# Performance work log

Measured on AMD Instinct MI355X. Metric: run time of the kernel, lower is better.

## Reference

```python
import jax, jax.numpy as jnp
import numpy as np

HIDDEN = 256
HORIZON = 24
FMET = 16
OUT = 1
EPS = 1e-5


def setup_inputs() -> dict:
    key = jax.random.key(0)
    ks = jax.random.split(key, 12)
    B, N = 16, 1000
    final_h = jax.random.normal(ks[0], (B, N, HIDDEN), dtype=jnp.float32)
    future_met = jax.random.normal(ks[1], (B, HORIZON, N, FMET), dtype=jnp.float32)
    # step_queries: xavier_uniform over (max_horizon, hidden)
    lim_q = float(np.sqrt(6.0 / (HORIZON + HIDDEN)))
    step_queries = jax.random.uniform(ks[2], (HORIZON, HIDDEN), minval=-lim_q, maxval=lim_q, dtype=jnp.float32)
    # future_met_proj: Linear(FMET -> HIDDEN); store weight as (FMET, HIDDEN)
    lim_fm = float(np.sqrt(1.0 / FMET))
    W_fm = jax.random.uniform(ks[3], (FMET, HIDDEN), minval=-lim_fm, maxval=lim_fm, dtype=jnp.float32)
    b_fm = jax.random.uniform(ks[4], (HIDDEN,), minval=-lim_fm, maxval=lim_fm, dtype=jnp.float32)
    gamma = jnp.ones((HIDDEN,), dtype=jnp.float32)
    beta = jnp.zeros((HIDDEN,), dtype=jnp.float32)
    lim1 = float(np.sqrt(1.0 / HIDDEN))
    W1 = jax.random.uniform(ks[5], (HIDDEN, HIDDEN), minval=-lim1, maxval=lim1, dtype=jnp.float32)
    b1 = jax.random.uniform(ks[6], (HIDDEN,), minval=-lim1, maxval=lim1, dtype=jnp.float32)
    W2 = jax.random.uniform(ks[7], (HIDDEN, OUT), minval=-lim1, maxval=lim1, dtype=jnp.float32)
    b2 = jax.random.uniform(ks[8], (OUT,), minval=-lim1, maxval=lim1, dtype=jnp.float32)
    return {
        "final_h": final_h,
        "future_met": future_met,
        "step_queries": step_queries,
        "W_fm": W_fm,
        "b_fm": b_fm,
        "gamma": gamma,
        "beta": beta,
        "W1": W1,
        "b1": b1,
        "W2": W2,
        "b2": b2,
    }


def _layer_norm(x, gamma, beta):
    mu = jnp.mean(x, axis=-1, keepdims=True)
    var = jnp.mean(jnp.square(x - mu), axis=-1, keepdims=True)
    return (x - mu) * jax.lax.rsqrt(var + EPS) * gamma + beta


def reference(final_h, future_met, step_queries, W_fm, b_fm, gamma, beta, W1, b1, W2, b2):
    # final_h: (B, N, H); future_met: (B, T, N, F)
    # combined: (B, N, T, H) = broadcast(final_h) + queries + proj(future_met)
    combined = final_h[:, :, None, :] + step_queries[None, None, :, :]
    fm = jnp.transpose(future_met, (0, 2, 1, 3))  # (B, N, T, F)
    combined = combined + (jnp.einsum("bntf,fh->bnth", fm, W_fm) + b_fm)
    x = _layer_norm(combined, gamma, beta)
    x = jax.nn.gelu(x @ W1 + b1, approximate=False)
    # dropout is identity in eval mode
    out = x @ W2 + b2  # (B, N, T, OUT)
    return jnp.transpose(out, (0, 2, 1, 3))  # (B, T, N, OUT)
```

## Files before the change

### kernel.cpp

```cpp
#include <hip/hip_runtime.h>
#include <hip/hip_bf16.h>
#include <stdint.h>

#define MROWS 32
#define LDA   264
#define FMS   40

typedef __bf16 bf16x8 __attribute__((ext_vector_type(8)));
typedef float  f32x4  __attribute__((ext_vector_type(4)));
typedef float  f32x2  __attribute__((ext_vector_type(2)));

__device__ __forceinline__ unsigned short f2bf(float f) {
    union { float f; uint32_t u; } v; v.f = f;
    return (unsigned short)((v.u + 0x7FFFu + ((v.u >> 16) & 1u)) >> 16);
}

__device__ __forceinline__ ushort2 pk_bf16(float a, float b) {
    union { __hip_bfloat162 v; ushort2 u; } c;
    c.v = __float22bfloat162_rn(make_float2(a, b));
    return c.u;
}

template <int CTRL>
__device__ __forceinline__ float dpp_radd(float x) {
    union { float f; int i; } a, b;
    a.f = x;
    b.i = __builtin_amdgcn_update_dpp(0, a.i, CTRL, 0xF, 0xF, true);
    return x + b.f;
}
#define ROW_SHR1 0x111
#define ROW_SHR2 0x112
#define ROW_SHR4 0x114
#define ROW_SHR8 0x118
__device__ __forceinline__ float dpp_rowsum(float x) {
    x = dpp_radd<ROW_SHR1>(x);
    x = dpp_radd<ROW_SHR2>(x);
    x = dpp_radd<ROW_SHR4>(x);
    x = dpp_radd<ROW_SHR8>(x);
    return x;
}

__device__ __forceinline__ f32x2 gelu_fast2(f32x2 v) {
    const f32x2 t = v * v;
    f32x2 p = t * 0.044715f + 1.0f;
    const f32x2 u = v * p;
    f32x2 e;
    e.x = __builtin_amdgcn_exp2f(u.x * -2.3021131160186336f);
    e.y = __builtin_amdgcn_exp2f(u.y * -2.3021131160186336f);
    f32x2 r;
    r.x = __builtin_amdgcn_rcpf(1.0f + e.x);
    r.y = __builtin_amdgcn_rcpf(1.0f + e.y);
    return v * r;
}

__device__ __forceinline__ int frag_n(int f) {
    return (f & 0xC0) | ((f & 3) << 4) | ((f >> 2) & 15);
}

__global__ __launch_bounds__(256) void prep1(const float* __restrict__ W1,
                                             const float* __restrict__ step_q,
                                             const float* __restrict__ b_fm,
                                             const float* __restrict__ W_fm,
                                             const float* __restrict__ gamma,
                                             const float* __restrict__ beta,
                                             unsigned short* __restrict__ w1frag,
                                             float* __restrict__ sqb,
                                             unsigned short* __restrict__ wfmfrag,
                                             float* __restrict__ gpart,
                                             float* __restrict__ bpart,
                                             float* __restrict__ WFWp,
                                             float* __restrict__ SQWp) {
    __shared__ unsigned short T[256][40];
    __shared__ float redw[8][32][41];
    const int blk = blockIdx.x, tid = threadIdx.x;
    if (blk < 8) {
        const int kk = blk;
        float sg = 0.f, sb = 0.f;
        #pragma unroll
        for (int r = 0; r < 32; ++r) {
            const int klog = frag_n((kk << 5) + r);
            const float wv = W1[klog * 256 + tid];
            const float gv = gamma[klog];
            sg = fmaf(gv, wv, sg);
            sb = fmaf(beta[klog], wv, sb);
            T[tid][r] = f2bf(wv * gv);
        }
        gpart[(kk << 8) + tid] = sg;
        bpart[(kk << 8) + tid] = sb;
        __syncthreads();
        #pragma unroll
        for (int f = 0; f < 4; ++f) {
            const int fi = (f << 8) + tid;
            const int l = fi & 63, j = (fi >> 6) & 3, w = fi >> 8;
            const int n = (w << 6) + (j << 4) + (l & 15);
            const uint4 v = *(const uint4*)&T[n][(l >> 4) << 3];
            *(uint4*)&w1frag[((w << 5) + (j << 3) + kk) * 512 + (l << 3)] = v;
        }
    } else if (blk < 32) {
        const int t = blk - 8;
        const int n = frag_n(tid);
        sqb[t * 256 + tid] = step_q[t * 256 + n] + b_fm[n];
    } else if (blk < 36) {
        const int f  = blk - 32;
        const int fr = (f << 8) + tid;
        const int l = fr & 63, j = (fr >> 6) & 3, w = fr >> 8;
        const int n = (w << 6) + (j << 4) + (l & 15);
        const int qr = l >> 4;
        #pragma unroll
        for (int e = 0; e < 8; ++e) {
            const int k = (qr << 3) + e;
            wfmfrag[(fr << 3) + e] = (k < 16) ? f2bf(W_fm[(k << 8) + n]) : (unsigned short)0;
        }
    } else {
        const int kc = tid >> 5, cl = tid & 31;
        const int n  = ((blk - 36) << 5) + cl;
        float wfw[16];
        float sqw[24];
        #pragma unroll
        for (int f = 0; f < 16; ++f) wfw[f] = 0.f;
        #pragma unroll
        for (int t = 0; t < 24; ++t) sqw[t] = 0.f;
        for (int hh = 0; hh < 32; ++hh) {
            const int h = (kc << 5) + hh;
            const float g1 = gamma[h] * W1[(h << 8) + n];
            #pragma unroll
            for (int f = 0; f < 16; ++f)
                wfw[f] = fmaf(W_fm[(f << 8) + h], g1, wfw[f]);
            const float bf = b_fm[h];
            #pragma unroll
            for (int t = 0; t < 24; ++t)
                sqw[t] = fmaf(step_q[(t << 8) + h] + bf, g1, sqw[t]);
        }
        #pragma unroll
        for (int f = 0; f < 16; ++f) redw[kc][cl][f] = wfw[f];
        #pragma unroll
        for (int t = 0; t < 24; ++t) redw[kc][cl][16 + t] = sqw[t];
        __syncthreads();
        for (int e = tid; e < 1280; e += 256) {
            const int cl2 = e & 31, v = e >> 5;
            float s = 0.f;
            #pragma unroll
            for (int k2 = 0; k2 < 8; ++k2) s += redw[k2][cl2][v];
            const int nn = ((blk - 36) << 5) + cl2;
            if (v < 16) WFWp[(v << 8) + nn] = s;
            else        SQWp[((v - 16) << 8) + nn] = s;
        }
    }
}

__global__ __launch_bounds__(256) void prep2(const float* __restrict__ gpart,
                                             const float* __restrict__ bpart,
                                             const float* __restrict__ b1,
                                             const float* __restrict__ W2,
                                             float* __restrict__ gw1f,
                                             float* __restrict__ b1tf,
                                             float* __restrict__ w2f) {
    const int tid = threadIdx.x;
    const int n = frag_n(tid);
    float sg = 0.f, sb = 0.f;
    #pragma unroll
    for (int kk = 0; kk < 8; ++kk) {
        sg += gpart[(kk << 8) + n];
        sb += bpart[(kk << 8) + n];
    }
    gw1f[tid] = sg;
    b1tf[tid] = sb + b1[n];
    w2f[tid]  = W2[n];
}

__global__ __launch_bounds__(256) void prep3(const float* __restrict__ final_h,
                                             const unsigned short* __restrict__ w1frag,
                                             const float* __restrict__ gpart,
                                             const float* __restrict__ bpart,
                                             const float* __restrict__ b1,
                                             const float* __restrict__ W2,
                                             const float* __restrict__ WFWp,
                                             const float* __restrict__ SQWp,
                                             float* __restrict__ gw1f,
                                             float* __restrict__ b1tf,
                                             float* __restrict__ w2f,
                                             unsigned short* __restrict__ wfwfrag,
                                             float* __restrict__ sqwf,
                                             float* __restrict__ FHW) {
    __shared__ __align__(16) unsigned short Abuf[MROWS * LDA];
    const int blk = blockIdx.x, tid = threadIdx.x;
    if (blk == 500) {
        const int n = frag_n(tid);
        float sg = 0.f, sb = 0.f;
        #pragma unroll
        for (int kk = 0; kk < 8; ++kk) {
            sg += gpart[(kk << 8) + n];
            sb += bpart[(kk << 8) + n];
        }
        gw1f[tid] = sg;
        b1tf[tid] = sb + b1[n];
        w2f[tid]  = W2[n];
        #pragma unroll
        for (int f = 0; f < 4; ++f) {
            const int fr = (f << 8) + tid;
            const int l = fr & 63, j = (fr >> 6) & 3, wq = fr >> 8;
            const int nn = (wq << 6) + (j << 4) + (l & 15);
            const int qr2 = l >> 4;
            #pragma unroll
            for (int e = 0; e < 8; ++e) {
                const int k = (qr2 << 3) + e;
                wfwfrag[(fr << 3) + e] = (k < 16) ? f2bf(WFWp[(k << 8) + nn]) : (unsigned short)0;
            }
        }
        #pragma unroll
        for (int t = 0; t < 24; ++t)
            sqwf[(t << 8) + tid] = SQWp[(t << 8) + n];
        return;
    }
    const int w = tid >> 6, l = tid & 63;
    const int col = l & 15, qr = l >> 4;
    const int fb = (w << 6) + (col << 2);
    const int R0 = blk << 5;
    #pragma unroll
    for (int i = 0; i < 2; ++i) {
        #pragma unroll
        for (int r = 0; r < 4; ++r) {
            const int m = (i << 4) + (qr << 2) + r;
            const float* src = final_h + ((R0 + m) << 8) + (w << 6) + col;
            const ushort2 p01 = pk_bf16(src[0],  src[16]);
            const ushort2 p23 = pk_bf16(src[32], src[48]);
            ushort4 o; o.x = p01.x; o.y = p01.y; o.z = p23.x; o.w = p23.y;
            *(ushort4*)&Abuf[m * LDA + fb] = o;
        }
    }
    __syncthreads();
    f32x4 acc[2][4];
    #pragma unroll
    for (int i = 0; i < 2; ++i)
        #pragma unroll
        for (int j = 0; j < 4; ++j)
            acc[i][j] = (f32x4){0.f, 0.f, 0.f, 0.f};
    {
        const unsigned short* Bw  = w1frag + (w << 14) + (l << 3);
        const unsigned short* Ab0 = &Abuf[col * LDA + (qr << 3)];
        const unsigned short* Ab1 = &Abuf[(16 + col) * LDA + (qr << 3)];
        #pragma unroll
        for (int kk = 0; kk < 8; ++kk) {
            const bf16x8 a0 = *(const bf16x8*)(Ab0 + (kk << 5));
            const bf16x8 a1 = *(const bf16x8*)(Ab1 + (kk << 5));
            #pragma unroll
            for (int j = 0; j < 4; ++j) {
                const bf16x8 bf = *(const bf16x8*)(Bw + (j << 12) + (kk << 9));
                acc[0][j] = __builtin_amdgcn_mfma_f32_16x16x32_bf16(a0, bf, acc[0][j], 0, 0, 0);
                acc[1][j] = __builtin_amdgcn_mfma_f32_16x16x32_bf16(a1, bf, acc[1][j], 0, 0, 0);
            }
        }
    }
    #pragma unroll
    for (int i = 0; i < 2; ++i) {
        #pragma unroll
        for (int r = 0; r < 4; ++r) {
            const int m = (i << 4) + (qr << 2) + r;
            float4 st;
            st.x = acc[i][0][r]; st.y = acc[i][1][r];
            st.z = acc[i][2][r]; st.w = acc[i][3][r];
            *(float4*)&FHW[((R0 + m) << 8) + fb] = st;
        }
    }
}

__global__ __launch_bounds__(256, 6) void fused_head(
    const float* __restrict__ final_h, const float* __restrict__ future_met,
    const float* __restrict__ b2,      const float* __restrict__ sqb,
    const unsigned short* __restrict__ wfmfrag,
    const float* __restrict__ gw1f,    const float* __restrict__ b1tf,
    const float* __restrict__ w2f,     const unsigned short* __restrict__ wfwfrag,
    const float* __restrict__ sqwf,    const float* __restrict__ FHW,
    float* __restrict__ out)
{
    __shared__ __align__(16) unsigned short fmA[MROWS * FMS];
    __shared__ float2 red[4][MROWS];
    __shared__ float2 mv[MROWS];
    __shared__ float  part[4][MROWS];

    const int tid = threadIdx.x;
    const int w   = tid >> 6;
    const int l   = tid & 63;
    const int col = l & 15;
    const int qr  = l >> 4;
    const int m0  = blockIdx.x * MROWS;
    const int bn0 = m0 / 24;
    const int tt0 = m0 - bn0 * 24;
    const int fb  = (w << 6) + (col << 2);

    if (tid < 128) {
        const int row = tid >> 2, f0 = (tid & 3) << 2;
        const int tta = tt0 + row;
        const int sub = (tta >= 24) + (tta >= 48);
        const int tt  = tta - sub * 24;
        const int bn  = bn0 + sub;
        const int b   = bn / 1000, n = bn - b * 1000;
        const float4 v = *(const float4*)&future_met[((((b * 24 + tt) * 1000) + n) << 4) + f0];
        ushort2 lo = pk_bf16(v.x, v.y), hi = pk_bf16(v.z, v.w);
        ushort4 o; o.x = lo.x; o.y = lo.y; o.z = hi.x; o.w = hi.y;
        *(ushort4*)&fmA[row * FMS + f0] = o;
    }
    {
        const int row = tid >> 3, k = 16 + ((tid & 7) << 1);
        *(unsigned int*)&fmA[row * FMS + k] = 0u;
    }
    __syncthreads();

    const int dlo = qr << 2;
    const int slo = ((tt0 + dlo) >= 24) + ((tt0 + dlo) >= 48);
    const int shi = ((tt0 + dlo + 19) >= 24) + ((tt0 + dlo + 19) >= 48);
    float flo[4], fhi[4];
    {
        const float* fhl = final_h + ((bn0 + slo) << 8) + (w << 6) + col;
        const float* fhh = final_h + ((bn0 + shi) << 8) + (w << 6) + col;
        #pragma unroll
        for (int j = 0; j < 4; ++j) { flo[j] = fhl[j << 4]; fhi[j] = fhh[j << 4]; }
    }

    f32x4 acc[2][4];
    #pragma unroll
    for (int i = 0; i < 2; ++i) {
        #pragma unroll
        for (int r = 0; r < 4; ++r) {
            const int d   = (i << 4) + (qr << 2) + r;
            const int tta = tt0 + d;
            const int sub = (tta >= 24) + (tta >= 48);
            const int tt  = tta - sub * 24;
            const bool lo = (sub == slo);
            const float4 sb4 = *(const float4*)&sqb[(tt << 8) + fb];
            acc[i][0][r] = (lo ? flo[0] : fhi[0]) + sb4.x;
            acc[i][1][r] = (lo ? flo[1] : fhi[1]) + sb4.y;
            acc[i][2][r] = (lo ? flo[2] : fhi[2]) + sb4.z;
            acc[i][3][r] = (lo ? flo[3] : fhi[3]) + sb4.w;
        }
    }
    const bf16x8 af0 = *(const bf16x8*)&fmA[col * FMS + (qr << 3)];
    const bf16x8 af1 = *(const bf16x8*)&fmA[(16 + col) * FMS + (qr << 3)];
    {
        const unsigned short* Bwf = wfmfrag + (w << 11) + (l << 3);
        #pragma unroll
        for (int j = 0; j < 4; ++j) {
            const bf16x8 bf = *(const bf16x8*)(Bwf + (j << 9));
            acc[0][j] = __builtin_amdgcn_mfma_f32_16x16x32_bf16(af0, bf, acc[0][j], 0, 0, 0);
            acc[1][j] = __builtin_amdgcn_mfma_f32_16x16x32_bf16(af1, bf, acc[1][j], 0, 0, 0);
        }
    }

    #pragma unroll
    for (int i = 0; i < 2; ++i) {
        #pragma unroll
        for (int r = 0; r < 4; ++r) {
            const int m = (i << 4) + (qr << 2) + r;
            const f32x2 vA = {acc[i][0][r], acc[i][1][r]};
            const f32x2 vB = {acc[i][2][r], acc[i][3][r]};
            const f32x2 sv = vA + vB;
            const f32x2 qv = vA * vA + vB * vB;
            float s = sv.x + sv.y;
            float q = qv.x + qv.y;
            s = dpp_rowsum(s);
            q = dpp_rowsum(q);
            if (col == 15) red[w][m] = make_float2(s, q);
        }
    }
    __syncthreads();

    if (tid < MROWS) {
        const float2 a0 = red[0][tid], a1 = red[1][tid], a2 = red[2][tid], a3 = red[3][tid];
        const float S = a0.x + a1.x + a2.x + a3.x;
        const float Q = a0.y + a1.y + a2.y + a3.y;
        const float mu = S * 0.00390625f;
        const float rstd = rsqrtf(Q * 0.00390625f - mu * mu + 1e-5f);
        mv[tid] = make_float2(mu, rstd);
    }

    #pragma unroll
    for (int i = 0; i < 2; ++i) {
        #pragma unroll
        for (int r = 0; r < 4; ++r) {
            const int d   = (i << 4) + (qr << 2) + r;
            const int tta = tt0 + d;
            const int sub = (tta >= 24) + (tta >= 48);
            const int tt  = tta - sub * 24;
            const float4 fw = *(const float4*)&FHW[((bn0 + sub) << 8) + fb];
            const float4 sw = *(const float4*)&sqwf[(tt << 8) + fb];
            acc[i][0][r] = fw.x + sw.x;
            acc[i][1][r] = fw.y + sw.y;
            acc[i][2][r] = fw.z + sw.z;
            acc[i][3][r] = fw.w + sw.w;
        }
    }
    {
        const unsigned short* Bw2 = wfwfrag + (w << 11) + (l << 3);
        #pragma unroll
        for (int j = 0; j < 4; ++j) {
            const bf16x8 bfv = *(const bf16x8*)(Bw2 + (j << 9));
            acc[0][j] = __builtin_amdgcn_mfma_f32_16x16x32_bf16(af0, bfv, acc[0][j], 0, 0, 0);
            acc[1][j] = __builtin_amdgcn_mfma_f32_16x16x32_bf16(af1, bfv, acc[1][j], 0, 0, 0);
        }
    }

    const float4 gw4 = *(const float4*)&gw1f[fb];
    const float4 bt4 = *(const float4*)&b1tf[fb];
    const float4 w24 = *(const float4*)&w2f[fb];
    const f32x2 gwA = {gw4.x, gw4.y}, gwB = {gw4.z, gw4.w};
    const f32x2 btA = {bt4.x, bt4.y}, btB = {bt4.z, bt4.w};
    const f32x2 w2A = {w24.x, w24.y}, w2B = {w24.z, w24.w};
    __syncthreads();

    #pragma unroll
    for (int i = 0; i < 2; ++i) {
        #pragma unroll
        for (int r = 0; r < 4; ++r) {
            const int m = (i << 4) + (qr << 2) + r;
            const float2 p = mv[m];
            const float cm = -p.x * p.y;
            const f32x2 baseA = gwA * cm + btA;
            const f32x2 baseB = gwB * cm + btB;
            const f32x2 accA = {acc[i][0][r], acc[i][1][r]};
            const f32x2 accB = {acc[i][2][r], acc[i][3][r]};
            const f32x2 yA = accA * p.y + baseA;
            const f32x2 yB = accB * p.y + baseB;
            const f32x2 gvA = gelu_fast2(yA);
            const f32x2 gvB = gelu_fast2(yB);
            const f32x2 pp2 = gvA * w2A + gvB * w2B;
            float pp = pp2.x + pp2.y;
            pp = dpp_rowsum(pp);
            if (col == 15) part[w][m] = pp;
        }
    }
    __syncthreads();

    if (tid < MROWS) {
        const int m = m0 + tid;
        const float val = part[0][tid] + part[1][tid] + part[2][tid] + part[3][tid] + b2[0];
        const int bn = m / 24, tt = m - bn * 24;
        const int b  = bn / 1000, n = bn - b * 1000;
        out[(b * 24 + tt) * 1000 + n] = val;
    }
}

__global__ __launch_bounds__(256, 6) void fused_head_v3(
    const float* __restrict__ final_h, const float* __restrict__ future_met,
    const float* __restrict__ b2,      const unsigned short* __restrict__ w1frag,
    const float* __restrict__ sqb,     const unsigned short* __restrict__ wfmfrag,
    const float* __restrict__ gw1f,    const float* __restrict__ b1tf,
    const float* __restrict__ w2f,     float* __restrict__ out)
{
    __shared__ __align__(16) unsigned short Abuf[MROWS * LDA];
    __shared__ __align__(16) unsigned short fmA[MROWS * FMS];
    __shared__ float2 red[4][MROWS];
    __shared__ float2 mv[MROWS];
    __shared__ float  part[4][MROWS];

    const int tid = threadIdx.x;
    const int w   = tid >> 6;
    const int l   = tid & 63;
    const int col = l & 15;
    const int qr  = l >> 4;
    const int m0  = blockIdx.x * MROWS;
    const int bn0 = m0 / 24;
    const int tt0 = m0 - bn0 * 24;
    const int fb  = (w << 6) + (col << 2);

    if (tid < 128) {
        const int row = tid >> 2, f0 = (tid & 3) << 2;
        const int tta = tt0 + row;
        const int sub = (tta >= 24) + (tta >= 48);
        const int tt  = tta - sub * 24;
        const int bn  = bn0 + sub;
        const int b   = bn / 1000, n = bn - b * 1000;
        const float4 v = *(const float4*)&future_met[((((b * 24 + tt) * 1000) + n) << 4) + f0];
        ushort2 lo = pk_bf16(v.x, v.y), hi = pk_bf16(v.z, v.w);
        ushort4 o; o.x = lo.x; o.y = lo.y; o.z = hi.x; o.w = hi.y;
        *(ushort4*)&fmA[row * FMS + f0] = o;
    }
    {
        const int row = tid >> 3, k = 16 + ((tid & 7) << 1);
        *(unsigned int*)&fmA[row * FMS + k] = 0u;
    }
    __syncthreads();

    const int dlo = qr << 2;
    const int slo = ((tt0 + dlo) >= 24) + ((tt0 + dlo) >= 48);
    const int shi = ((tt0 + dlo + 19) >= 24) + ((tt0 + dlo + 19) >= 48);
    float flo[4], fhi[4];
    {
        const float* fhl = final_h + ((bn0 + slo) << 8) + (w << 6) + col;
        const float* fhh = final_h + ((bn0 + shi) << 8) + (w << 6) + col;
        #pragma unroll
        for (int j = 0; j < 4; ++j) { flo[j] = fhl[j << 4]; fhi[j] = fhh[j << 4]; }
    }

    f32x4 acc[2][4];
    #pragma unroll
    for (int i = 0; i < 2; ++i) {
        #pragma unroll
        for (int r = 0; r < 4; ++r) {
            const int d   = (i << 4) + (qr << 2) + r;
            const int tta = tt0 + d;
            const int sub = (tta >= 24) + (tta >= 48);
            const int tt  = tta - sub * 24;
            const bool lo = (sub == slo);
            const float4 sb4 = *(const float4*)&sqb[(tt << 8) + fb];
            acc[i][0][r] = (lo ? flo[0] : fhi[0]) + sb4.x;
            acc[i][1][r] = (lo ? flo[1] : fhi[1]) + sb4.y;
            acc[i][2][r] = (lo ? flo[2] : fhi[2]) + sb4.z;
            acc[i][3][r] = (lo ? flo[3] : fhi[3]) + sb4.w;
        }
    }
    {
        const bf16x8 af0 = *(const bf16x8*)&fmA[col * FMS + (qr << 3)];
        const bf16x8 af1 = *(const bf16x8*)&fmA[(16 + col) * FMS + (qr << 3)];
        const unsigned short* Bwf = wfmfrag + (w << 11) + (l << 3);
        #pragma unroll
        for (int j = 0; j < 4; ++j) {
            const bf16x8 bf = *(const bf16x8*)(Bwf + (j << 9));
            acc[0][j] = __builtin_amdgcn_mfma_f32_16x16x32_bf16(af0, bf, acc[0][j], 0, 0, 0);
            acc[1][j] = __builtin_amdgcn_mfma_f32_16x16x32_bf16(af1, bf, acc[1][j], 0, 0, 0);
        }
    }

    #pragma unroll
    for (int i = 0; i < 2; ++i) {
        #pragma unroll
        for (int r = 0; r < 4; ++r) {
            const int m = (i << 4) + (qr << 2) + r;
            const f32x2 vA = {acc[i][0][r], acc[i][1][r]};
            const f32x2 vB = {acc[i][2][r], acc[i][3][r]};
            const f32x2 sv = vA + vB;
            const f32x2 qv = vA * vA + vB * vB;
            float s = sv.x + sv.y;
            float q = qv.x + qv.y;
            const ushort2 p01 = pk_bf16(vA.x, vA.y);
            const ushort2 p23 = pk_bf16(vB.x, vB.y);
            s = dpp_rowsum(s);
            q = dpp_rowsum(q);
            if (col == 15) red[w][m] = make_float2(s, q);
            ushort4 o; o.x = p01.x; o.y = p01.y; o.z = p23.x; o.w = p23.y;
            *(ushort4*)&Abuf[m * LDA + (w << 6) + (col << 2)] = o;
        }
    }
    __syncthreads();

    if (tid < MROWS) {
        const float2 a0 = red[0][tid], a1 = red[1][tid], a2 = red[2][tid], a3 = red[3][tid];
        const float S = a0.x + a1.x + a2.x + a3.x;
        const float Q = a0.y + a1.y + a2.y + a3.y;
        const float mu = S * 0.00390625f;
        const float rstd = rsqrtf(Q * 0.00390625f - mu * mu + 1e-5f);
        mv[tid] = make_float2(mu, rstd);
    }

    #pragma unroll
    for (int i = 0; i < 2; ++i)
        #pragma unroll
        for (int j = 0; j < 4; ++j)
            acc[i][j] = (f32x4){0.f, 0.f, 0.f, 0.f};

    {
        const unsigned short* Bw  = w1frag + (w << 14) + (l << 3);
        const unsigned short* Ab0 = &Abuf[col * LDA + (qr << 3)];
        const unsigned short* Ab1 = &Abuf[(16 + col) * LDA + (qr << 3)];
        #pragma unroll
        for (int kk = 0; kk < 8; ++kk) {
            const bf16x8 a0 = *(const bf16x8*)(Ab0 + (kk << 5));
            const bf16x8 a1 = *(const bf16x8*)(Ab1 + (kk << 5));
            #pragma unroll
            for (int j = 0; j < 4; ++j) {
                const bf16x8 bf = *(const bf16x8*)(Bw + (j << 12) + (kk << 9));
                acc[0][j] = __builtin_amdgcn_mfma_f32_16x16x32_bf16(a0, bf, acc[0][j], 0, 0, 0);
                acc[1][j] = __builtin_amdgcn_mfma_f32_16x16x32_bf16(a1, bf, acc[1][j], 0, 0, 0);
            }
        }
    }

    const float4 gw4 = *(const float4*)&gw1f[fb];
    const float4 bt4 = *(const float4*)&b1tf[fb];
    const float4 w24 = *(const float4*)&w2f[fb];
    const f32x2 gwA = {gw4.x, gw4.y}, gwB = {gw4.z, gw4.w};
    const f32x2 btA = {bt4.x, bt4.y}, btB = {bt4.z, bt4.w};
    const f32x2 w2A = {w24.x, w24.y}, w2B = {w24.z, w24.w};
    __syncthreads();

    #pragma unroll
    for (int i = 0; i < 2; ++i) {
        #pragma unroll
        for (int r = 0; r < 4; ++r) {
            const int m = (i << 4) + (qr << 2) + r;
            const float2 p = mv[m];
            const float cm = -p.x * p.y;
            const f32x2 baseA = gwA * cm + btA;
            const f32x2 baseB = gwB * cm + btB;
            const f32x2 accA = {acc[i][0][r], acc[i][1][r]};
            const f32x2 accB = {acc[i][2][r], acc[i][3][r]};
            const f32x2 yA = accA * p.y + baseA;
            const f32x2 yB = accB * p.y + baseB;
            const f32x2 gvA = gelu_fast2(yA);
            const f32x2 gvB = gelu_fast2(yB);
            const f32x2 pp2 = gvA * w2A + gvB * w2B;
            float pp = pp2.x + pp2.y;
            pp = dpp_rowsum(pp);
            if (col == 15) part[w][m] = pp;
        }
    }
    __syncthreads();

    if (tid < MROWS) {
        const int m = m0 + tid;
        const float val = part[0][tid] + part[1][tid] + part[2][tid] + part[3][tid] + b2[0];
        const int bn = m / 24, tt = m - bn * 24;
        const int b  = bn / 1000, n = bn - b * 1000;
        out[(b * 24 + tt) * 1000 + n] = val;
    }
}

extern "C" void kernel_launch(void* const* d_in, const int* in_sizes, int n_in,
                              void* d_out, int out_size, void* d_ws, size_t ws_size,
                              hipStream_t stream) {
    const float* final_h    = (const float*)d_in[0];
    const float* future_met = (const float*)d_in[1];
    const float* step_q     = (const float*)d_in[2];
    const float* W_fm       = (const float*)d_in[3];
    const float* b_fm       = (const float*)d_in[4];
    const float* gamma      = (const float*)d_in[5];
    const float* beta       = (const float*)d_in[6];
    const float* W1         = (const float*)d_in[7];
    const float* b1         = (const float*)d_in[8];
    const float* W2         = (const float*)d_in[9];
    const float* b2         = (const float*)d_in[10];

    char* ws = (char*)d_ws;
    unsigned short* w1frag  = (unsigned short*)(ws);
    float*          sqb     = (float*)(ws + 131072);
    unsigned short* wfmfrag = (unsigned short*)(ws + 155648);
    float*          gpart   = (float*)(ws + 172032);
    float*          bpart   = (float*)(ws + 180224);
    float*          gw1f    = (float*)(ws + 188416);
    float*          b1tf    = (float*)(ws + 189440);
    float*          w2f     = (float*)(ws + 190464);
    float*          WFWp    = (float*)(ws + 191488);
    float*          SQWp    = (float*)(ws + 207872);
    unsigned short* wfwfrag = (unsigned short*)(ws + 232448);
    float*          sqwf    = (float*)(ws + 248832);
    float*          FHW     = (float*)(ws + 274432);
    float* out = (float*)d_out;

    const size_t WS_NEEDED = 274432u + 16384000u;
    if (ws_size >= WS_NEEDED) {
        prep1<<<44, 256, 0, stream>>>(W1, step_q, b_fm, W_fm, gamma, beta,
                                      w1frag, sqb, wfmfrag, gpart, bpart, WFWp, SQWp);
        prep3<<<501, 256, 0, stream>>>(final_h, w1frag, gpart, bpart, b1, W2,
                                       WFWp, SQWp, gw1f, b1tf, w2f,
                                       wfwfrag, sqwf, FHW);
        fused_head<<<12000, 256, 0, stream>>>(final_h, future_met, b2, sqb, wfmfrag,
                                              gw1f, b1tf, w2f, wfwfrag, sqwf, FHW, out);
    } else {
        prep1<<<36, 256, 0, stream>>>(W1, step_q, b_fm, W_fm, gamma, beta,
                                      w1frag, sqb, wfmfrag, gpart, bpart, WFWp, SQWp);
        prep2<<<1, 256, 0, stream>>>(gpart, bpart, b1, W2, gw1f, b1tf, w2f);
        fused_head_v3<<<12000, 256, 0, stream>>>(final_h, future_met, b2, w1frag, sqb,
                                                 wfmfrag, gw1f, b1tf, w2f, out);
    }
}
```

Baseline: 225.3 us.

## Merge prep kernels into one launch computing W1 fragments inline

```diff
diff --git a/kernel.cpp b/kernel.cpp
--- a/kernel.cpp
+++ b/kernel.cpp
@@ -7,6 +7,7 @@
 #define FMS   40
 
 typedef __bf16 bf16x8 __attribute__((ext_vector_type(8)));
+typedef unsigned short u16x8 __attribute__((ext_vector_type(8)));
 typedef float  f32x4  __attribute__((ext_vector_type(4)));
 typedef float  f32x2  __attribute__((ext_vector_type(2)));
 
@@ -56,52 +57,88 @@
 __device__ __forceinline__ int frag_n(int f) {
     return (f & 0xC0) | ((f & 3) << 4) | ((f >> 2) & 15);
 }
-
-__global__ __launch_bounds__(256) void prep1(const float* __restrict__ W1,
-                                             const float* __restrict__ step_q,
-                                             const float* __restrict__ b_fm,
-                                             const float* __restrict__ W_fm,
-                                             const float* __restrict__ gamma,
-                                             const float* __restrict__ beta,
-                                             unsigned short* __restrict__ w1frag,
-                                             float* __restrict__ sqb,
-                                             unsigned short* __restrict__ wfmfrag,
-                                             float* __restrict__ gpart,
-                                             float* __restrict__ bpart,
-                                             float* __restrict__ WFWp,
-                                             float* __restrict__ SQWp) {
-    __shared__ unsigned short T[256][40];
-    __shared__ float redw[8][32][41];
+__device__ __forceinline__ int frag_inv(int n) {
+    return (n & 0xC0) | ((n & 15) << 2) | ((n >> 4) & 3);
+}
+
+__global__ __launch_bounds__(256) void prep_all(
+    const float* __restrict__ final_h, const float* __restrict__ W1,
+    const float* __restrict__ step_q,  const float* __restrict__ b_fm,
+    const float* __restrict__ W_fm,    const float* __restrict__ gamma,
+    const float* __restrict__ beta,    const float* __restrict__ b1,
+    const float* __restrict__ W2,
+    float* __restrict__ sqb,           unsigned short* __restrict__ wfmfrag,
+    float* __restrict__ gw1f,          float* __restrict__ b1tf,
+    float* __restrict__ w2f,           unsigned short* __restrict__ wfwfrag,
+    float* __restrict__ sqwf,          float* __restrict__ FHW)
+{
+    __shared__ __align__(16) unsigned char smem[MROWS * LDA * 2];
     const int blk = blockIdx.x, tid = threadIdx.x;
-    if (blk < 8) {
-        const int kk = blk;
-        float sg = 0.f, sb = 0.f;
-        #pragma unroll
-        for (int r = 0; r < 32; ++r) {
-            const int klog = frag_n((kk << 5) + r);
-            const float wv = W1[klog * 256 + tid];
-            const float gv = gamma[klog];
-            sg = fmaf(gv, wv, sg);
-            sb = fmaf(beta[klog], wv, sb);
-            T[tid][r] = f2bf(wv * gv);
-        }
-        gpart[(kk << 8) + tid] = sg;
-        bpart[(kk << 8) + tid] = sb;
+
+    if (blk < 500) {
+        unsigned short* Abuf = (unsigned short*)smem;
+        const int w = tid >> 6, l = tid & 63;
+        const int col = l & 15, qr = l >> 4;
+        const int R0 = blk << 5;
+        #pragma unroll
+        for (int i = 0; i < 2; ++i) {
+            #pragma unroll
+            for (int r = 0; r < 4; ++r) {
+                const int m = (i << 4) + (qr << 2) + r;
+                const float* src = final_h + ((R0 + m) << 8) + (w << 6) + col;
+                unsigned short* Ab = &Abuf[m * LDA + (w << 6) + col];
+                const ushort2 p01 = pk_bf16(src[0],  src[16]);
+                const ushort2 p23 = pk_bf16(src[32], src[48]);
+                Ab[0] = p01.x; Ab[16] = p01.y; Ab[32] = p23.x; Ab[48] = p23.y;
+            }
+        }
         __syncthreads();
-        #pragma unroll
-        for (int f = 0; f < 4; ++f) {
-            const int fi = (f << 8) + tid;
-            const int l = fi & 63, j = (fi >> 6) & 3, w = fi >> 8;
-            const int n = (w << 6) + (j << 4) + (l & 15);
-            const uint4 v = *(const uint4*)&T[n][(l >> 4) << 3];
-            *(uint4*)&w1frag[((w << 5) + (j << 3) + kk) * 512 + (l << 3)] = v;
-        }
-    } else if (blk < 32) {
-        const int t = blk - 8;
+        f32x4 acc[2][4];
+        #pragma unroll
+        for (int i = 0; i < 2; ++i)
+            #pragma unroll
+            for (int j = 0; j < 4; ++j)
+                acc[i][j] = (f32x4){0.f, 0.f, 0.f, 0.f};
+        const int nb = (w << 6) + col;
+        #pragma unroll
+        for (int kk = 0; kk < 8; ++kk) {
+            const int k0 = (kk << 5) + (qr << 3);
+            float g[8];
+            #pragma unroll
+            for (int e = 0; e < 8; ++e) g[e] = gamma[k0 + e];
+            const bf16x8 a0 = *(const bf16x8*)&Abuf[col * LDA + k0];
+            const bf16x8 a1 = *(const bf16x8*)&Abuf[(16 + col) * LDA + k0];
+            #pragma unroll
+            for (int j = 0; j < 4; ++j) {
+                const float* wp = W1 + k0 * 256 + nb + (j << 4);
+                const ushort2 c0 = pk_bf16(wp[0]    * g[0], wp[256]  * g[1]);
+                const ushort2 c1 = pk_bf16(wp[512]  * g[2], wp[768]  * g[3]);
+                const ushort2 c2 = pk_bf16(wp[1024] * g[4], wp[1280] * g[5]);
+                const ushort2 c3 = pk_bf16(wp[1536] * g[6], wp[1792] * g[7]);
+                union { u16x8 u; bf16x8 b; } bv;
+                bv.u[0] = c0.x; bv.u[1] = c0.y; bv.u[2] = c1.x; bv.u[3] = c1.y;
+                bv.u[4] = c2.x; bv.u[5] = c2.y; bv.u[6] = c3.x; bv.u[7] = c3.y;
+                acc[0][j] = __builtin_amdgcn_mfma_f32_16x16x32_bf16(a0, bv.b, acc[0][j], 0, 0, 0);
+                acc[1][j] = __builtin_amdgcn_mfma_f32_16x16x32_bf16(a1, bv.b, acc[1][j], 0, 0, 0);
+            }
+        }
+        #pragma unroll
+        for (int i = 0; i < 2; ++i) {
+            #pragma unroll
+            for (int r = 0; r < 4; ++r) {
+                const int m = (i << 4) + (qr << 2) + r;
+                float4 st;
+                st.x = acc[i][0][r]; st.y = acc[i][1][r];
+                st.z = acc[i][2][r]; st.w = acc[i][3][r];
+                *(float4*)&FHW[((R0 + m) << 8) + (w << 6) + (col << 2)] = st;
+            }
+        }
+    } else if (blk < 524) {
+        const int t = blk - 500;
         const int n = frag_n(tid);
         sqb[t * 256 + tid] = step_q[t * 256 + n] + b_fm[n];
-    } else if (blk < 36) {
-        const int f  = blk - 32;
+    } else if (blk < 528) {
+        const int f  = blk - 524;
         const int fr = (f << 8) + tid;
         const int l = fr & 63, j = (fr >> 6) & 3, w = fr >> 8;
         const int n = (w << 6) + (j << 4) + (l & 15);
@@ -111,156 +148,59 @@
             const int k = (qr << 3) + e;
             wfmfrag[(fr << 3) + e] = (k < 16) ? f2bf(W_fm[(k << 8) + n]) : (unsigned short)0;
         }
-    } else {
-        const int kc = tid >> 5, cl = tid & 31;
-        const int n  = ((blk - 36) << 5) + cl;
-        float wfw[16];
-        float sqw[24];
-        #pragma unroll
-        for (int f = 0; f < 16; ++f) wfw[f] = 0.f;
-        #pragma unroll
-        for (int t = 0; t < 24; ++t) sqw[t] = 0.f;
-        for (int hh = 0; hh < 32; ++hh) {
-            const int h = (kc << 5) + hh;
-            const float g1 = gamma[h] * W1[(h << 8) + n];
-            #pragma unroll
-            for (int f = 0; f < 16; ++f)
-                wfw[f] = fmaf(W_fm[(f << 8) + h], g1, wfw[f]);
-            const float bf = b_fm[h];
-            #pragma unroll
-            for (int t = 0; t < 24; ++t)
-                sqw[t] = fmaf(step_q[(t << 8) + h] + bf, g1, sqw[t]);
-        }
-        #pragma unroll
-        for (int f = 0; f < 16; ++f) redw[kc][cl][f] = wfw[f];
-        #pragma unroll
-        for (int t = 0; t < 24; ++t) redw[kc][cl][16 + t] = sqw[t];
-        __syncthreads();
-        for (int e = tid; e < 1280; e += 256) {
-            const int cl2 = e & 31, v = e >> 5;
-            float s = 0.f;
-            #pragma unroll
-            for (int k2 = 0; k2 < 8; ++k2) s += redw[k2][cl2][v];
-            const int nn = ((blk - 36) << 5) + cl2;
-            if (v < 16) WFWp[(v << 8) + nn] = s;
-            else        SQWp[((v - 16) << 8) + nn] = s;
-        }
-    }
-}
-
-__global__ __launch_bounds__(256) void prep2(const float* __restrict__ gpart,
-                                             const float* __restrict__ bpart,
-                                             const float* __restrict__ b1,
-                                             const float* __restrict__ W2,
-                                             float* __restrict__ gw1f,
-                                             float* __restrict__ b1tf,
-                                             float* __restrict__ w2f) {
-    const int tid = threadIdx.x;
-    const int n = frag_n(tid);
-    float sg = 0.f, sb = 0.f;
-    #pragma unroll
-    for (int kk = 0; kk < 8; ++kk) {
-        sg += gpart[(kk << 8) + n];
-        sb += bpart[(kk << 8) + n];
-    }
-    gw1f[tid] = sg;
-    b1tf[tid] = sb + b1[n];
-    w2f[tid]  = W2[n];
-}
-
-__global__ __launch_bounds__(256) void prep3(const float* __restrict__ final_h,
-                                             const unsigned short* __restrict__ w1frag,
-                                             const float* __restrict__ gpart,
-                                             const float* __restrict__ bpart,
-                                             const float* __restrict__ b1,
-                                             const float* __restrict__ W2,
-                                             const float* __restrict__ WFWp,
-                                             const float* __restrict__ SQWp,
-                                             float* __restrict__ gw1f,
-                                             float* __restrict__ b1tf,
-                                             float* __restrict__ w2f,
-                                             unsigned short* __restrict__ wfwfrag,
-                                             float* __restrict__ sqwf,
-                                             float* __restrict__ FHW) {
-    __shared__ __align__(16) unsigned short Abuf[MROWS * LDA];
-    const int blk = blockIdx.x, tid = threadIdx.x;
-    if (blk == 500) {
+    } else if (blk == 528) {
         const int n = frag_n(tid);
         float sg = 0.f, sb = 0.f;
-        #pragma unroll
-        for (int kk = 0; kk < 8; ++kk) {
-            sg += gpart[(kk << 8) + n];
-            sb += bpart[(kk << 8) + n];
+        for (int k = 0; k < 256; ++k) {
+            const float wv = W1[(k << 8) + n];
+            sg = fmaf(gamma[k], wv, sg);
+            sb = fmaf(beta[k],  wv, sb);
         }
         gw1f[tid] = sg;
         b1tf[tid] = sb + b1[n];
         w2f[tid]  = W2[n];
-        #pragma unroll
-        for (int f = 0; f < 4; ++f) {
-            const int fr = (f << 8) + tid;
+    } else if (blk == 529) {
+        float* WFWs = (float*)smem;
+        float wfw[16];
+        #pragma unroll
+        for (int f = 0; f < 16; ++f) wfw[f] = 0.f;
+        for (int h = 0; h < 256; ++h) {
+            const float g1 = gamma[h] * W1[(h << 8) + tid];
+            #pragma unroll
+            for (int f = 0; f < 16; ++f)
+                wfw[f] = fmaf(W_fm[(f << 8) + h], g1, wfw[f]);
+        }
+        #pragma unroll
+        for (int f = 0; f < 16; ++f) WFWs[(f << 8) + tid] = wfw[f];
+        __syncthreads();
+        #pragma unroll
+        for (int ff = 0; ff < 4; ++ff) {
+            const int fr = (ff << 8) + tid;
             const int l = fr & 63, j = (fr >> 6) & 3, wq = fr >> 8;
             const int nn = (wq << 6) + (j << 4) + (l & 15);
             const int qr2 = l >> 4;
             #pragma unroll
             for (int e = 0; e < 8; ++e) {
                 const int k = (qr2 << 3) + e;
-                wfwfrag[(fr << 3) + e] = (k < 16) ? f2bf(WFWp[(k << 8) + nn]) : (unsigned short)0;
+                wfwfrag[(fr << 3) + e] = (k < 16) ? f2bf(WFWs[(k << 8) + nn]) : (unsigned short)0;
             }
         }
+    } else {
+        float sqw[24];
+        #pragma unroll
+        for (int t = 0; t < 24; ++t) sqw[t] = 0.f;
+        float bsum = 0.f;
+        for (int h = 0; h < 256; ++h) {
+            const float g1 = gamma[h] * W1[(h << 8) + tid];
+            bsum = fmaf(b_fm[h], g1, bsum);
+            #pragma unroll
+            for (int t = 0; t < 24; ++t)
+                sqw[t] = fmaf(step_q[(t << 8) + h], g1, sqw[t]);
+        }
+        const int fpos = frag_inv(tid);
         #pragma unroll
         for (int t = 0; t < 24; ++t)
-            sqwf[(t << 8) + tid] = SQWp[(t << 8) + n];
-        return;
-    }
-    const int w = tid >> 6, l = tid & 63;
-    const int col = l & 15, qr = l >> 4;
-    const int fb = (w << 6) + (col << 2);
-    const int R0 = blk << 5;
-    #pragma unroll
-    for (int i = 0; i < 2; ++i) {
-        #pragma unroll
-        for (int r = 0; r < 4; ++r) {
-            const int m = (i << 4) + (qr << 2) + r;
-            const float* src = final_h + ((R0 + m) << 8) + (w << 6) + col;
-            const ushort2 p01 = pk_bf16(src[0],  src[16]);
-            const ushort2 p23 = pk_bf16(src[32], src[48]);
-            ushort4 o; o.x = p01.x; o.y = p01.y; o.z = p23.x; o.w = p23.y;
-            *(ushort4*)&Abuf[m * LDA + fb] = o;
-        }
-    }
-    __syncthreads();
-    f32x4 acc[2][4];
-    #pragma unroll
-    for (int i = 0; i < 2; ++i)
-        #pragma unroll
-        for (int j = 0; j < 4; ++j)
-            acc[i][j] = (f32x4){0.f, 0.f, 0.f, 0.f};
-    {
-        const unsigned short* Bw  = w1frag + (w << 14) + (l << 3);
-        const unsigned short* Ab0 = &Abuf[col * LDA + (qr << 3)];
-        const unsigned short* Ab1 = &Abuf[(16 + col) * LDA + (qr << 3)];
-        #pragma unroll
-        for (int kk = 0; kk < 8; ++kk) {
-            const bf16x8 a0 = *(const bf16x8*)(Ab0 + (kk << 5));
-            const bf16x8 a1 = *(const bf16x8*)(Ab1 + (kk << 5));
-            #pragma unroll
-            for (int j = 0; j < 4; ++j) {
-                const bf16x8 bf = *(const bf16x8*)(Bw + (j << 12) + (kk << 9));
-                acc[0][j] = __builtin_amdgcn_mfma_f32_16x16x32_bf16(a0, bf, acc[0][j], 0, 0, 0);
-                acc[1][j] = __builtin_amdgcn_mfma_f32_16x16x32_bf16(a1, bf, acc[1][j], 0, 0, 0);
-            }
-        }
-    }
-    #pragma unroll
-    for (int i = 0; i < 2; ++i) {
-        #pragma unroll
-        for (int r = 0; r < 4; ++r) {
-            const int m = (i << 4) + (qr << 2) + r;
-            float4 st;
-            st.x = acc[i][0][r]; st.y = acc[i][1][r];
-            st.z = acc[i][2][r]; st.w = acc[i][3][r];
-            *(float4*)&FHW[((R0 + m) << 8) + fb] = st;
-        }
+            sqwf[(t << 8) + fpos] = sqw[t] + bsum;
     }
 }
 
@@ -439,6 +379,80 @@
     }
 }
 
+__global__ __launch_bounds__(256) void prep1_fb(const float* __restrict__ W1,
+                                                const float* __restrict__ step_q,
+                                                const float* __restrict__ b_fm,
+                                                const float* __restrict__ W_fm,
+                                                const float* __restrict__ gamma,
+                                                const float* __restrict__ beta,
+                                                unsigned short* __restrict__ w1frag,
+                                                float* __restrict__ sqb,
+                                                unsigned short* __restrict__ wfmfrag,
+                                                float* __restrict__ gpart,
+                                                float* __restrict__ bpart) {
+    __shared__ unsigned short T[256][40];
+    const int blk = blockIdx.x, tid = threadIdx.x;
+    if (blk < 8) {
+        const int kk = blk;
+        float sg = 0.f, sb = 0.f;
+        #pragma unroll
+        for (int r = 0; r < 32; ++r) {
+            const int klog = frag_n((kk << 5) + r);
+            const float wv = W1[klog * 256 + tid];
+            const float gv = gamma[klog];
+            sg = fmaf(gv, wv, sg);
+            sb = fmaf(beta[klog], wv, sb);
+            T[tid][r] = f2bf(wv * gv);
+        }
+        gpart[(kk << 8) + tid] = sg;
+        bpart[(kk << 8) + tid] = sb;
+        __syncthreads();
+        #pragma unroll
+        for (int f = 0; f < 4; ++f) {
+            const int fi = (f << 8) + tid;
+            const int l = fi & 63, j = (fi >> 6) & 3, w = fi >> 8;
+            const int n = (w << 6) + (j << 4) + (l & 15);
+            const uint4 v = *(const uint4*)&T[n][(l >> 4) << 3];
+            *(uint4*)&w1frag[((w << 5) + (j << 3) + kk) * 512 + (l << 3)] = v;
+        }
+    } else if (blk < 32) {
+        const int t = blk - 8;
+        const int n = frag_n(tid);
+        sqb[t * 256 + tid] = step_q[t * 256 + n] + b_fm[n];
+    } else {
+        const int f  = blk - 32;
+        const int fr = (f << 8) + tid;
+        const int l = fr & 63, j = (fr >> 6) & 3, w = fr >> 8;
+        const int n = (w << 6) + (j << 4) + (l & 15);
+        const int qr = l >> 4;
+        #pragma unroll
+        for (int e = 0; e < 8; ++e) {
+            const int k = (qr << 3) + e;
+            wfmfrag[(fr << 3) + e] = (k < 16) ? f2bf(W_fm[(k << 8) + n]) : (unsigned short)0;
+        }
+    }
+}
+
+__global__ __launch_bounds__(256) void prep2_fb(const float* __restrict__ gpart,
+                                                const float* __restrict__ bpart,
+                                                const float* __restrict__ b1,
+                                                const float* __restrict__ W2,
+                                                float* __restrict__ gw1f,
+                                                float* __restrict__ b1tf,
+                                                float* __restrict__ w2f) {
+    const int tid = threadIdx.x;
+    const int n = frag_n(tid);
+    float sg = 0.f, sb = 0.f;
+    #pragma unroll
+    for (int kk = 0; kk < 8; ++kk) {
+        sg += gpart[(kk << 8) + n];
+        sb += bpart[(kk << 8) + n];
+    }
+    gw1f[tid] = sg;
+    b1tf[tid] = sb + b1[n];
+    w2f[tid]  = W2[n];
+}
+
 __global__ __launch_bounds__(256, 6) void fused_head_v3(
     const float* __restrict__ final_h, const float* __restrict__ future_met,
     const float* __restrict__ b2,      const unsigned short* __restrict__ w1frag,
@@ -628,37 +642,38 @@
     const float* b1         = (const float*)d_in[8];
     const float* W2         = (const float*)d_in[9];
     const float* b2         = (const float*)d_in[10];
-
+    float* out = (float*)d_out;
     char* ws = (char*)d_ws;
-    unsigned short* w1frag  = (unsigned short*)(ws);
-    float*          sqb     = (float*)(ws + 131072);
-    unsigned short* wfmfrag = (unsigned short*)(ws + 155648);
-    float*          gpart   = (float*)(ws + 172032);
-    float*          bpart   = (float*)(ws + 180224);
-    float*          gw1f    = (float*)(ws + 188416);
-    float*          b1tf    = (float*)(ws + 189440);
-    float*          w2f     = (float*)(ws + 190464);
-    float*          WFWp    = (float*)(ws + 191488);
-    float*          SQWp    = (float*)(ws + 207872);
-    unsigned short* wfwfrag = (unsigned short*)(ws + 232448);
-    float*          sqwf    = (float*)(ws + 248832);
-    float*          FHW     = (float*)(ws + 274432);
-    float* out = (float*)d_out;
-
-    const size_t WS_NEEDED = 274432u + 16384000u;
+
+    float*          sqb     = (float*)(ws);
+    unsigned short* wfmfrag = (unsigned short*)(ws + 24576);
+    float*          gw1f    = (float*)(ws + 40960);
+    float*          b1tf    = (float*)(ws + 41984);
+    float*          w2f     = (float*)(ws + 43008);
+    unsigned short* wfwfrag = (unsigned short*)(ws + 44032);
+    float*          sqwf    = (float*)(ws + 60416);
+    float*          FHW     = (float*)(ws + 84992);
+    const size_t WS_NEEDED = 84992u + 16384000u;
+
     if (ws_size >= WS_NEEDED) {
-        prep1<<<44, 256, 0, stream>>>(W1, step_q, b_fm, W_fm, gamma, beta,
-                                      w1frag, sqb, wfmfrag, gpart, bpart, WFWp, SQWp);
-        prep3<<<501, 256, 0, stream>>>(final_h, w1frag, gpart, bpart, b1, W2,
-                                       WFWp, SQWp, gw1f, b1tf, w2f,
-                                       wfwfrag, sqwf, FHW);
+        prep_all<<<531, 256, 0, stream>>>(final_h, W1, step_q, b_fm, W_fm, gamma,
+                                          beta, b1, W2, sqb, wfmfrag,
+                                          gw1f, b1tf, w2f, wfwfrag, sqwf, FHW);
         fused_head<<<12000, 256, 0, stream>>>(final_h, future_met, b2, sqb, wfmfrag,
                                               gw1f, b1tf, w2f, wfwfrag, sqwf, FHW, out);
     } else {
-        prep1<<<36, 256, 0, stream>>>(W1, step_q, b_fm, W_fm, gamma, beta,
-                                      w1frag, sqb, wfmfrag, gpart, bpart, WFWp, SQWp);
-        prep2<<<1, 256, 0, stream>>>(gpart, bpart, b1, W2, gw1f, b1tf, w2f);
-        fused_head_v3<<<12000, 256, 0, stream>>>(final_h, future_met, b2, w1frag, sqb,
-                                                 wfmfrag, gw1f, b1tf, w2f, out);
-    }
-}
+        unsigned short* w1frag_f  = (unsigned short*)(ws);
+        float*          sqb_f     = (float*)(ws + 131072);
+        unsigned short* wfmfrag_f = (unsigned short*)(ws + 155648);
+        float*          gpart_f   = (float*)(ws + 172032);
+        float*          bpart_f   = (float*)(ws + 180224);
+        float*          gw1f_f    = (float*)(ws + 188416);
+        float*          b1tf_f    = (float*)(ws + 189440);
+        float*          w2f_f     = (float*)(ws + 190464);
+        prep1_fb<<<36, 256, 0, stream>>>(W1, step_q, b_fm, W_fm, gamma, beta,
+                                         w1frag_f, sqb_f, wfmfrag_f, gpart_f, bpart_f);
+        prep2_fb<<<1, 256, 0, stream>>>(gpart_f, bpart_f, b1, W2, gw1f_f, b1tf_f, w2f_f);
+        fused_head_v3<<<12000, 256, 0, stream>>>(final_h, future_met, b2, w1frag_f, sqb_f,
+                                                 wfmfrag_f, gw1f_f, b1tf_f, w2f_f, out);
+    }
+}
```

After: 243.1 us. 7.9% more time.
